# Kernel optimization log

Hardware: AMD Instinct MI355X
Metric: run time of the kernel (lower is better)

The kernel has to match this reference:

```python
import jax, jax.numpy as jnp
import numpy as np

N_NODES = 100000
N_EDGES = 1600000
D = 32
K = 3  # Chebyshev kernels
NEG_SLOPE = 0.2


def setup_inputs() -> dict:
    key = jax.random.key(0)
    ks = jax.random.split(key, 10)
    s = 1.0 / np.sqrt(D)
    return {
        "u": jax.random.normal(ks[0], (N_NODES, D), jnp.float32),
        "lambda_max": jnp.full((1,), 2.0, jnp.float32),
        "edge_src": jax.random.randint(ks[1], (N_EDGES,), 0, N_NODES, jnp.int32),
        "edge_dst": jax.random.randint(ks[2], (N_EDGES,), 0, N_NODES, jnp.int32),
        "cheb_W": jax.random.normal(ks[3], (K * D, D), jnp.float32) * s,
        "cheb_b": jnp.zeros((D,), jnp.float32),
        "src_W": jax.random.normal(ks[4], (D, D), jnp.float32) * s,
        "src_b": jnp.zeros((D,), jnp.float32),
        "dst_W": jax.random.normal(ks[5], (D, D), jnp.float32) * s,
        "dst_b": jnp.zeros((D,), jnp.float32),
        "attn": jax.random.normal(ks[6], (1, D), jnp.float32) * s,  # (heads=1, D)
    }


def reference(u, lambda_max, edge_src, edge_dst, cheb_W, cheb_b,
              src_W, src_b, dst_W, dst_b, attn):
    N = u.shape[0]
    # in-degrees (DGL: clamp(min=1) ** -0.5)
    deg = jnp.zeros((N,), u.dtype).at[edge_dst].add(1.0)
    Dinv = jnp.clip(deg, 1.0, None) ** -0.5  # (N,)

    def unnL(x):  # D^{-1/2} A D^{-1/2} x  via copy_u->sum message passing
        m = (x * Dinv[:, None])[edge_src]                       # (E, D)
        agg = jax.ops.segment_sum(m, edge_dst, num_segments=N)  # (N, D)
        return agg * Dinv[:, None]

    # --- ChebConv ---
    re_norm = 2.0 / lambda_max  # (1,) broadcast over all nodes
    X0 = u
    Xt = [X0]
    X1 = X0
    if K > 1:
        h = unnL(X0)
        X1 = -re_norm * h + X0 * (re_norm - 1.0)
        Xt.append(X1)
    for _ in range(2, K):
        h = unnL(X1)
        Xi = -2.0 * re_norm * h + X1 * (2.0 * (re_norm - 1.0)) - X0
        Xt.append(Xi)
        X0, X1 = X1, Xi
    Xcat = jnp.concatenate(Xt, axis=1)                 # (N, K*D)
    hc = jax.nn.relu(Xcat @ cheb_W + cheb_b)           # (N, D), DGL default activation=relu

    # --- GATv2Conv (heads=1) ---
    H = attn.shape[0]
    fsrc = (hc @ src_W + src_b).reshape(N, H, -1)      # (N, H, D)
    fdst = (hc @ dst_W + dst_b).reshape(N, H, -1)
    e = jax.nn.leaky_relu(fsrc[edge_src] + fdst[edge_dst], NEG_SLOPE)  # (E, H, D)
    logits = jnp.einsum('ehd,hd->eh', e, attn)         # (E, H)
    mx = jax.ops.segment_max(logits, edge_dst, num_segments=N)
    mx = jnp.where(jnp.isfinite(mx), mx, 0.0)
    ex = jnp.exp(logits - mx[edge_dst])
    den = jax.ops.segment_sum(ex, edge_dst, num_segments=N)
    a = ex / jnp.where(den > 0, den, 1.0)[edge_dst]    # edge softmax over dst groups
    msg = fsrc[edge_src] * a[:, :, None]               # (E, H, D)
    out = jax.ops.segment_sum(msg, edge_dst, num_segments=N)  # (N, H, D)
    return out.squeeze(1)
```

## Files before the change

### kernel.cpp

```cpp
#include <hip/hip_runtime.h>
#include <hip/hip_bf16.h>


typedef unsigned short u16;

#define DD 32
#define NEG_SLOPE 0.2f
#define BLK 256
#define TILE 4096
#define CB_SHIFT 8
#define CB_NODES 256
#define SRC_BITS 17

#define OFF_CHEBW 0
#define OFF_CHEBB 3072
#define OFF_SRCW  3104
#define OFF_SRCB  4128
#define OFF_DSTW  4160
#define OFF_DSTB  5184
#define OFF_ATTN  5216
#define OFF_LMAX  5248
#define W_TOTAL   5249

#define F_U     0
#define F_CHEBW 1
#define F_CHEBB 2
#define F_SRCW  3
#define F_SRCB  4
#define F_DSTW  5
#define F_DSTB  6
#define F_ATTN  7
#define F_LMAX  8
#define N_FLAGS 9

__device__ __forceinline__ float bh2f(u16 h) {
    return __uint_as_float(((unsigned)h) << 16);
}
__device__ __forceinline__ float rdin(const void* p, long long i, int f32f) {
    return f32f ? ((const float*)p)[i] : bh2f(((const u16*)p)[i]);
}
__device__ __forceinline__ float4 rd4(const void* p, long long row, int q, int f32f) {
    if (f32f) return ((const float4*)p)[row * 8 + q];
    ushort4 h = ((const ushort4*)p)[row * 8 + q];
    return make_float4(bh2f(h.x), bh2f(h.y), bh2f(h.z), bh2f(h.w));
}
__device__ __forceinline__ float lrelu(float x) { return fmaxf(x, NEG_SLOPE * x); }

__device__ __forceinline__ int plaus(u16 h) {
    if ((h & 0x7FFFu) == 0) return 1;
    unsigned e = (h >> 7) & 0xFF;
    return (e >= 0x60 && e <= 0x8F) ? 1 : 0;
}

__global__ void k_detect(const void* p0, const void* p1, const void* p2,
                         const void* p3, const void* p4, const void* p5,
                         const void* p6, const void* p7, const void* p8,
                         int n0, int n7, int* __restrict__ flags) {
    __shared__ int cEven, cEvenZ, cOddNZ;
    const void* ptrs[N_FLAGS] = {p0, p1, p2, p3, p4, p5, p6, p7, p8};
    const int   ns[N_FLAGS]   = {n0, 3072, 32, 1024, 32, 1024, 32, n7, 1};
    int a = blockIdx.x;
    if (a >= N_FLAGS) return;
    const u16* h = (const u16*)ptrs[a];
    int n = ns[a];
    if (threadIdx.x == 0) { cEven = 0; cEvenZ = 0; cOddNZ = 0; }
    __syncthreads();
    if (n == 1) {
        if (threadIdx.x == 0) {
            u16 v = h[0];
            flags[a] = ((v & 0x7FFFu) == 0 || !plaus(v)) ? 1 : 0;
        }
        return;
    }
    int nprobe = n >> 1;
    if (nprobe > 64) nprobe = 64;
    int t = threadIdx.x;
    if (t < nprobe) {
        u16 ev = h[2 * t];
        u16 od = h[2 * t + 1];
        if (plaus(ev)) atomicAdd(&cEven, 1);
        if ((ev & 0x7FFFu) == 0) atomicAdd(&cEvenZ, 1);
        if (plaus(od) && (od & 0x7FFFu) != 0) atomicAdd(&cOddNZ, 1);
    }
    __syncthreads();
    if (threadIdx.x == 0) {
        int bf = (cEven * 4 >= nprobe * 3);
        if (cEvenZ == nprobe && cOddNZ * 2 >= nprobe) bf = 0;
        flags[a] = bf ? 0 : 1;
    }
}

__global__ void k_cvtw(const void* chebW, const void* chebB, const void* srcW,
                       const void* srcB, const void* dstW, const void* dstB,
                       const void* attn, const void* lmax,
                       const int* __restrict__ flags, float* __restrict__ wsW,
                       unsigned* __restrict__ Mabs) {
    int i = blockIdx.x * blockDim.x + threadIdx.x;
    if (i >= W_TOTAL + 32) return;
    if (i >= W_TOTAL) { Mabs[i - W_TOTAL] = 0u; return; }
    float v;
    if      (i < OFF_CHEBB) v = rdin(chebW, i - OFF_CHEBW, flags[F_CHEBW]);
    else if (i < OFF_SRCW)  v = rdin(chebB, i - OFF_CHEBB, flags[F_CHEBB]);
    else if (i < OFF_SRCB)  v = rdin(srcW,  i - OFF_SRCW,  flags[F_SRCW]);
    else if (i < OFF_DSTW)  v = rdin(srcB,  i - OFF_SRCB,  flags[F_SRCB]);
    else if (i < OFF_DSTB)  v = rdin(dstW,  i - OFF_DSTW,  flags[F_DSTW]);
    else if (i < OFF_ATTN)  v = rdin(dstB,  i - OFF_DSTB,  flags[F_DSTB]);
    else if (i < OFF_LMAX)  v = rdin(attn,  i - OFF_ATTN,  flags[F_ATTN]);
    else                    v = rdin(lmax,  0,             flags[F_LMAX]);
    wsW[i] = v;
}


__global__ __launch_bounds__(BLK) void k_h1(
        const int* __restrict__ dst, unsigned* __restrict__ hist1,
        int E, int T, int NB1) {
    __shared__ unsigned lh[512];
    int tile = blockIdx.x, t = threadIdx.x;
    for (int b = t; b < 512; b += BLK) lh[b] = 0;
    __syncthreads();
    int base = tile * TILE;
    for (int i = 0; i < TILE / BLK; i++) {
        int e = base + i * BLK + t;
        if (e < E) atomicAdd(&lh[dst[e] >> CB_SHIFT], 1u);
    }
    __syncthreads();
    for (int b = t; b < NB1; b += BLK) hist1[(size_t)b * T + tile] = lh[b];
}

__global__ __launch_bounds__(BLK) void k_scA(
        unsigned* __restrict__ h, unsigned* __restrict__ bsum, int T) {
    __shared__ unsigned s[BLK];
    int b = blockIdx.x, t = threadIdx.x;
    unsigned carry = 0;
    for (int base = 0; base < T; base += BLK) {
        int i = base + t;
        unsigned v = (i < T) ? h[(size_t)b * T + i] : 0u;
        s[t] = v;
        __syncthreads();
        for (int off = 1; off < BLK; off <<= 1) {
            unsigned a = (t >= off) ? s[t - off] : 0u;
            __syncthreads();
            s[t] += a;
            __syncthreads();
        }
        if (i < T) h[(size_t)b * T + i] = carry + s[t] - v;
        carry += s[BLK - 1];
        __syncthreads();
    }
    if (t == 0) bsum[b] = carry;
}

__global__ __launch_bounds__(512) void k_scB(
        unsigned* __restrict__ bsum, int NB1,
        unsigned* __restrict__ row_ptr, int N, int E) {
    __shared__ unsigned s[512];
    int t = threadIdx.x;
    unsigned v = (t < NB1) ? bsum[t] : 0u;
    s[t] = v;
    __syncthreads();
    for (int off = 1; off < 512; off <<= 1) {
        unsigned a = (t >= off) ? s[t - off] : 0u;
        __syncthreads();
        s[t] += a;
        __syncthreads();
    }
    if (t < NB1) bsum[t] = s[t] - v;
    if (t == 0) row_ptr[N] = (unsigned)E;
}

__global__ __launch_bounds__(BLK) void k_s1(
        const int* __restrict__ src, const int* __restrict__ dst,
        const unsigned* __restrict__ off1, const unsigned* __restrict__ bsum,
        unsigned* __restrict__ tmp, int E, int T, int NB1) {
    __shared__ unsigned cur[512];
    int tile = blockIdx.x, t = threadIdx.x;
    for (int b = t; b < NB1; b += BLK)
        cur[b] = off1[(size_t)b * T + tile] + bsum[b];
    __syncthreads();
    int base = tile * TILE;
    for (int i = 0; i < TILE / BLK; i++) {
        int e = base + i * BLK + t;
        if (e < E) {
            int d = dst[e];
            unsigned pos = atomicAdd(&cur[d >> CB_SHIFT], 1u);
            tmp[pos] = ((unsigned)(d & (CB_NODES - 1)) << SRC_BITS) | (unsigned)src[e];
        }
    }
}

__global__ __launch_bounds__(BLK) void k_p2(
        const unsigned* __restrict__ tmp, const unsigned* __restrict__ bsum,
        unsigned* __restrict__ row_ptr, float* __restrict__ dinv,
        int* __restrict__ srcs, int N, int E, int T, int NB1) {
    __shared__ unsigned hist[CB_NODES], cur[CB_NODES], ssc[BLK];
    int b = blockIdx.x, t = threadIdx.x;
    int nodeBase = b << CB_SHIFT;
    unsigned lo = bsum[b];
    unsigned hi = (b + 1 < NB1) ? bsum[b + 1] : (unsigned)E;
    hist[t] = 0;
    __syncthreads();
    for (unsigned e = lo + t; e < hi; e += BLK)
        atomicAdd(&hist[tmp[e] >> SRC_BITS], 1u);
    __syncthreads();
    unsigned v = hist[t];
    ssc[t] = v;
    __syncthreads();
    for (int off = 1; off < BLK; off <<= 1) {
        unsigned a = (t >= off) ? ssc[t - off] : 0u;
        __syncthreads();
        ssc[t] += a;
        __syncthreads();
    }
    unsigned ex = ssc[t] - v;
    cur[t] = ex;
    int node = nodeBase + t;
    if (node < N) {
        row_ptr[node] = lo + ex;
        unsigned c = v;
        if (c < 1u) c = 1u;
        dinv[node] = rsqrtf((float)c);
    }
    __syncthreads();
    for (unsigned e = lo + t; e < hi; e += BLK) {
        unsigned p = tmp[e];
        unsigned pos = lo + atomicAdd(&cur[p >> SRC_BITS], 1u);
        srcs[pos] = (int)(p & ((1u << SRC_BITS) - 1u));
    }
}


__global__ __launch_bounds__(BLK) void k_unnl1(
        const void* __restrict__ u, const int* __restrict__ flags,
        const float* __restrict__ dinv, const unsigned* __restrict__ row_ptr,
        const int* __restrict__ srcs, const float* __restrict__ wsW,
        float* __restrict__ X1, int N) {
    int wave = (blockIdx.x * BLK + threadIdx.x) >> 6;
    if (wave >= N) return;
    int lane = threadIdx.x & 63, q = lane & 7, g = lane >> 3;
    int f = flags[F_U];
    int base = (int)row_ptr[wave], end = (int)row_ptr[wave + 1];
    float4 acc = make_float4(0.f, 0.f, 0.f, 0.f);
    for (int i = base; i < end; i += 32) {
        int e0 = i + g, e1 = i + 8 + g, e2 = i + 16 + g, e3 = i + 24 + g;
        int s0 = srcs[min(e0, end - 1)], s1 = srcs[min(e1, end - 1)];
        int s2 = srcs[min(e2, end - 1)], s3 = srcs[min(e3, end - 1)];
        float dv0 = dinv[s0], dv1 = dinv[s1], dv2 = dinv[s2], dv3 = dinv[s3];
        if (e0 >= end) dv0 = 0.f;
        if (e1 >= end) dv1 = 0.f;
        if (e2 >= end) dv2 = 0.f;
        if (e3 >= end) dv3 = 0.f;
        float4 x0 = rd4(u, s0, q, f);
        float4 x1 = rd4(u, s1, q, f);
        float4 x2 = rd4(u, s2, q, f);
        float4 x3 = rd4(u, s3, q, f);
        acc.x += x0.x * dv0 + x1.x * dv1 + x2.x * dv2 + x3.x * dv3;
        acc.y += x0.y * dv0 + x1.y * dv1 + x2.y * dv2 + x3.y * dv3;
        acc.z += x0.z * dv0 + x1.z * dv1 + x2.z * dv2 + x3.z * dv3;
        acc.w += x0.w * dv0 + x1.w * dv1 + x2.w * dv2 + x3.w * dv3;
    }
#pragma unroll
    for (int off = 8; off <= 32; off <<= 1) {
        acc.x += __shfl_xor(acc.x, off);
        acc.y += __shfl_xor(acc.y, off);
        acc.z += __shfl_xor(acc.z, off);
        acc.w += __shfl_xor(acc.w, off);
    }
    if (g == 0) {
        float rn = 2.0f / wsW[OFF_LMAX];
        float dn = dinv[wave];
        float4 x0 = rd4(u, wave, q, f);
        float4 r;
        r.x = -rn * (acc.x * dn) + x0.x * (rn - 1.f);
        r.y = -rn * (acc.y * dn) + x0.y * (rn - 1.f);
        r.z = -rn * (acc.z * dn) + x0.z * (rn - 1.f);
        r.w = -rn * (acc.w * dn) + x0.w * (rn - 1.f);
        ((float4*)X1)[(size_t)wave * 8 + q] = r;
    }
}

__global__ __launch_bounds__(BLK) void k_unnl2(
        const void* __restrict__ u, const int* __restrict__ flags,
        const float* __restrict__ X1, const float* __restrict__ dinv,
        const unsigned* __restrict__ row_ptr, const int* __restrict__ srcs,
        const float* __restrict__ wsW, float* __restrict__ X2, int N) {
    int wave = (blockIdx.x * BLK + threadIdx.x) >> 6;
    if (wave >= N) return;
    int lane = threadIdx.x & 63, q = lane & 7, g = lane >> 3;
    int base = (int)row_ptr[wave], end = (int)row_ptr[wave + 1];
    float4 acc = make_float4(0.f, 0.f, 0.f, 0.f);
    for (int i = base; i < end; i += 32) {
        int e0 = i + g, e1 = i + 8 + g, e2 = i + 16 + g, e3 = i + 24 + g;
        int s0 = srcs[min(e0, end - 1)], s1 = srcs[min(e1, end - 1)];
        int s2 = srcs[min(e2, end - 1)], s3 = srcs[min(e3, end - 1)];
        float dv0 = dinv[s0], dv1 = dinv[s1], dv2 = dinv[s2], dv3 = dinv[s3];
        if (e0 >= end) dv0 = 0.f;
        if (e1 >= end) dv1 = 0.f;
        if (e2 >= end) dv2 = 0.f;
        if (e3 >= end) dv3 = 0.f;
        float4 x0 = ((const float4*)X1)[(size_t)s0 * 8 + q];
        float4 x1 = ((const float4*)X1)[(size_t)s1 * 8 + q];
        float4 x2 = ((const float4*)X1)[(size_t)s2 * 8 + q];
        float4 x3 = ((const float4*)X1)[(size_t)s3 * 8 + q];
        acc.x += x0.x * dv0 + x1.x * dv1 + x2.x * dv2 + x3.x * dv3;
        acc.y += x0.y * dv0 + x1.y * dv1 + x2.y * dv2 + x3.y * dv3;
        acc.z += x0.z * dv0 + x1.z * dv1 + x2.z * dv2 + x3.z * dv3;
        acc.w += x0.w * dv0 + x1.w * dv1 + x2.w * dv2 + x3.w * dv3;
    }
#pragma unroll
    for (int off = 8; off <= 32; off <<= 1) {
        acc.x += __shfl_xor(acc.x, off);
        acc.y += __shfl_xor(acc.y, off);
        acc.z += __shfl_xor(acc.z, off);
        acc.w += __shfl_xor(acc.w, off);
    }
    if (g == 0) {
        float rn = 2.0f / wsW[OFF_LMAX];
        float dn = dinv[wave];
        float4 x0 = rd4(u, wave, q, flags[F_U]);
        float4 x1 = ((const float4*)X1)[(size_t)wave * 8 + q];
        float4 r;
        r.x = -2.f * rn * (acc.x * dn) + x1.x * (2.f * (rn - 1.f)) - x0.x;
        r.y = -2.f * rn * (acc.y * dn) + x1.y * (2.f * (rn - 1.f)) - x0.y;
        r.z = -2.f * rn * (acc.z * dn) + x1.z * (2.f * (rn - 1.f)) - x0.z;
        r.w = -2.f * rn * (acc.w * dn) + x1.w * (2.f * (rn - 1.f)) - x0.w;
        ((float4*)X2)[(size_t)wave * 8 + q] = r;
    }
}

__global__ __launch_bounds__(BLK) void k_cfsd(
        const void* __restrict__ u, const int* __restrict__ flags,
        const float* __restrict__ X1, const float* __restrict__ X2,
        const float* __restrict__ wsW, float* __restrict__ fsrc,
        float* __restrict__ fdst, unsigned* __restrict__ Mabs, int N) {
    __shared__ float sW[3072], sWs[1024], sWd[1024];
    __shared__ float sb[32], sbs[32], sbd[32];
    __shared__ float hcS[BLK * 33];
    __shared__ unsigned mloc[32];
    int t = threadIdx.x;
    for (int i = t; i < 3072; i += BLK) sW[i] = wsW[OFF_CHEBW + i];
    for (int i = t; i < 1024; i += BLK) {
        sWs[i] = wsW[OFF_SRCW + i];
        sWd[i] = wsW[OFF_DSTW + i];
    }
    if (t < 32) {
        sb[t]  = wsW[OFF_CHEBB + t];
        sbs[t] = wsW[OFF_SRCB + t];
        sbd[t] = wsW[OFF_DSTB + t];
        mloc[t] = 0u;
    }
    __syncthreads();
    int f = flags[F_U];
    float mabs = 0.f;
    int n = blockIdx.x * BLK + t;
    if (n < N) {
        long long row = (long long)n;
        float acc[32];
#pragma unroll
        for (int j = 0; j < 32; j++) acc[j] = sb[j];
        for (int i4 = 0; i4 < 8; i4++) {
            float4 x = rd4(u, row, i4, f);
            const float* w = &sW[i4 * 128];
#pragma unroll
            for (int j = 0; j < 32; j++) acc[j] = fmaf(x.x, w[j], acc[j]);
#pragma unroll
            for (int j = 0; j < 32; j++) acc[j] = fmaf(x.y, w[32 + j], acc[j]);
#pragma unroll
            for (int j = 0; j < 32; j++) acc[j] = fmaf(x.z, w[64 + j], acc[j]);
#pragma unroll
            for (int j = 0; j < 32; j++) acc[j] = fmaf(x.w, w[96 + j], acc[j]);
        }
        for (int i4 = 0; i4 < 8; i4++) {
            float4 x = ((const float4*)X1)[row * 8 + i4];
            const float* w = &sW[1024 + i4 * 128];
#pragma unroll
            for (int j = 0; j < 32; j++) acc[j] = fmaf(x.x, w[j], acc[j]);
#pragma unroll
            for (int j = 0; j < 32; j++) acc[j] = fmaf(x.y, w[32 + j], acc[j]);
#pragma unroll
            for (int j = 0; j < 32; j++) acc[j] = fmaf(x.z, w[64 + j], acc[j]);
#pragma unroll
            for (int j = 0; j < 32; j++) acc[j] = fmaf(x.w, w[96 + j], acc[j]);
        }
        for (int i4 = 0; i4 < 8; i4++) {
            float4 x = ((const float4*)X2)[row * 8 + i4];
            const float* w = &sW[2048 + i4 * 128];
#pragma unroll
            for (int j = 0; j < 32; j++) acc[j] = fmaf(x.x, w[j], acc[j]);
#pragma unroll
            for (int j = 0; j < 32; j++) acc[j] = fmaf(x.y, w[32 + j], acc[j]);
#pragma unroll
            for (int j = 0; j < 32; j++) acc[j] = fmaf(x.z, w[64 + j], acc[j]);
#pragma unroll
            for (int j = 0; j < 32; j++) acc[j] = fmaf(x.w, w[96 + j], acc[j]);
        }
#pragma unroll
        for (int j = 0; j < 32; j++) hcS[t * 33 + j] = fmaxf(acc[j], 0.f);
        float as[32], ad[32];
#pragma unroll
        for (int j = 0; j < 32; j++) { as[j] = sbs[j]; ad[j] = sbd[j]; }
        for (int i = 0; i < 32; i++) {
            float hv = hcS[t * 33 + i];
            const float* ws = &sWs[i * 32];
            const float* wd = &sWd[i * 32];
#pragma unroll
            for (int j = 0; j < 32; j++) {
                as[j] = fmaf(hv, ws[j], as[j]);
                ad[j] = fmaf(hv, wd[j], ad[j]);
            }
        }
        float4* fs4 = (float4*)(fsrc + row * 32);
        float4* fd4 = (float4*)(fdst + row * 32);
#pragma unroll
        for (int i4 = 0; i4 < 8; i4++) {
            fs4[i4] = make_float4(as[4 * i4], as[4 * i4 + 1], as[4 * i4 + 2], as[4 * i4 + 3]);
            fd4[i4] = make_float4(ad[4 * i4], ad[4 * i4 + 1], ad[4 * i4 + 2], ad[4 * i4 + 3]);
        }
#pragma unroll
        for (int j = 0; j < 32; j++) mabs = fmaxf(mabs, fabsf(as[j]));
    }
    atomicMax(&mloc[t & 31], __float_as_uint(mabs));
    __syncthreads();
    if (t < 32) atomicMax(&Mabs[t], mloc[t]);
}

__global__ __launch_bounds__(BLK) void k_gat(
        const float* __restrict__ fsrc, const float* __restrict__ fdst,
        const unsigned* __restrict__ row_ptr, const int* __restrict__ srcs,
        const float* __restrict__ wsW, const unsigned* __restrict__ Mabs,
        float* __restrict__ out, int N) {
    int wave = (blockIdx.x * BLK + threadIdx.x) >> 6;
    if (wave >= N) return;
    int lane = threadIdx.x & 63, q = lane & 7, g = lane >> 3;
    int base = (int)row_ptr[wave], end = (int)row_ptr[wave + 1];
    if (base == end) {
        if (g == 0)
            ((float4*)out)[(size_t)wave * 8 + q] = make_float4(0.f, 0.f, 0.f, 0.f);
        return;
    }
    float4 fd = ((const float4*)fdst)[(size_t)wave * 8 + q];
    float4 at = ((const float4*)(wsW + OFF_ATTN))[q];
    float4 mb = ((const float4*)Mabs)[q];
    float kp = (mb.x + fabsf(fd.x)) * fabsf(at.x) +
               (mb.y + fabsf(fd.y)) * fabsf(at.y) +
               (mb.z + fabsf(fd.z)) * fabsf(at.z) +
               (mb.w + fabsf(fd.w)) * fabsf(at.w);
    kp += __shfl_xor(kp, 1);
    kp += __shfl_xor(kp, 2);
    kp += __shfl_xor(kp, 4);
    float K = kp;
    float4 acc = make_float4(0.f, 0.f, 0.f, 0.f);
    float den = 0.f;
    for (int i = base; i < end; i += 16) {
        int e0 = i + g, e1 = i + 8 + g;
        int ec0 = min(e0, end - 1), ec1 = min(e1, end - 1);
        int s0 = srcs[ec0], s1 = srcs[ec1];
        float4 fs0 = ((const float4*)fsrc)[(size_t)s0 * 8 + q];
        float4 fs1 = ((const float4*)fsrc)[(size_t)s1 * 8 + q];
        float v0 = lrelu(fs0.x + fd.x) * at.x + lrelu(fs0.y + fd.y) * at.y +
                   lrelu(fs0.z + fd.z) * at.z + lrelu(fs0.w + fd.w) * at.w;
        float v1 = lrelu(fs1.x + fd.x) * at.x + lrelu(fs1.y + fd.y) * at.y +
                   lrelu(fs1.z + fd.z) * at.z + lrelu(fs1.w + fd.w) * at.w;
        v0 += __shfl_xor(v0, 1);  v1 += __shfl_xor(v1, 1);
        v0 += __shfl_xor(v0, 2);  v1 += __shfl_xor(v1, 2);
        v0 += __shfl_xor(v0, 4);  v1 += __shfl_xor(v1, 4);
        float w0 = (e0 < end) ? __expf(v0 - K) : 0.f;
        float w1 = (e1 < end) ? __expf(v1 - K) : 0.f;
        acc.x += fs0.x * w0 + fs1.x * w1;
        acc.y += fs0.y * w0 + fs1.y * w1;
        acc.z += fs0.z * w0 + fs1.z * w1;
        acc.w += fs0.w * w0 + fs1.w * w1;
        den += w0 + w1;
    }
#pragma unroll
    for (int off = 8; off <= 32; off <<= 1) {
        acc.x += __shfl_xor(acc.x, off);
        acc.y += __shfl_xor(acc.y, off);
        acc.z += __shfl_xor(acc.z, off);
        acc.w += __shfl_xor(acc.w, off);
        den   += __shfl_xor(den, off);
    }
    if (g == 0) {
        float inv = 1.f / (den > 0.f ? den : 1.f);
        ((float4*)out)[(size_t)wave * 8 + q] =
            make_float4(acc.x * inv, acc.y * inv, acc.z * inv, acc.w * inv);
    }
}

extern "C" void kernel_launch(void* const* d_in, const int* in_sizes, int n_in,
                              void* d_out, int out_size, void* d_ws, size_t ws_size,
                              hipStream_t stream) {
    const void* u     = d_in[0];
    const void* lmax  = d_in[1];
    const int*  esrc  = (const int*)d_in[2];
    const int*  edst  = (const int*)d_in[3];
    const void* chebW = d_in[4];
    const void* chebB = d_in[5];
    const void* srcW  = d_in[6];
    const void* srcB  = d_in[7];
    const void* dstW  = d_in[8];
    const void* dstB  = d_in[9];
    const void* attn  = d_in[10];

    const int ND = in_sizes[0];
    const int N  = ND / DD;
    const int E  = in_sizes[2];

    const int NB1 = (N + CB_NODES - 1) >> CB_SHIFT;
    const int T   = (E + TILE - 1) / TILE;
    const int M   = NB1 * T;

    float* ws   = (float*)d_ws;
    float* X1   = ws;
    float* X2   = ws + (size_t)ND;
    unsigned* tmp = (unsigned*)(ws + 2 * (size_t)ND);
    int*   srcs = (int*)(tmp + E);
    unsigned* hist1   = (unsigned*)(srcs + E);
    unsigned* row_ptr = hist1 + M;
    float*    dinv    = (float*)(row_ptr + (N + 1));
    unsigned* bsum    = (unsigned*)(dinv + N);
    float*    wsW     = (float*)(((uintptr_t)(bsum + NB1) + 15) & ~(uintptr_t)15);
    int*      flags   = (int*)(wsW + W_TOTAL);
    unsigned* Mabs    = (unsigned*)(((uintptr_t)(flags + N_FLAGS) + 15) & ~(uintptr_t)15);
    float*    out     = (float*)d_out;

    auto gb = [](long long n, int b) { return (unsigned)((n + b - 1) / b); };

    k_detect<<<N_FLAGS, 64, 0, stream>>>(u, chebW, chebB, srcW, srcB, dstW, dstB,
                                         attn, lmax, ND, DD, flags);
    k_cvtw<<<gb(W_TOTAL + 32, BLK), BLK, 0, stream>>>(chebW, chebB, srcW, srcB,
                                                      dstW, dstB, attn, lmax,
                                                      flags, wsW, Mabs);

    k_h1<<<T, BLK, 0, stream>>>(edst, hist1, E, T, NB1);
    k_scA<<<NB1, BLK, 0, stream>>>(hist1, bsum, T);
    k_scB<<<1, 512, 0, stream>>>(bsum, NB1, row_ptr, N, E);
    k_s1<<<T, BLK, 0, stream>>>(esrc, edst, hist1, bsum, tmp, E, T, NB1);
    k_p2<<<NB1, BLK, 0, stream>>>(tmp, bsum, row_ptr, dinv, srcs, N, E, T, NB1);

    k_unnl1<<<gb((long long)N * 64, BLK), BLK, 0, stream>>>(u, flags, dinv, row_ptr,
                                                            srcs, wsW, X1, N);
    k_unnl2<<<gb((long long)N * 64, BLK), BLK, 0, stream>>>(u, flags, X1, dinv, row_ptr,
                                                            srcs, wsW, X2, N);

    k_cfsd<<<gb(N, BLK), BLK, 0, stream>>>(u, flags, X1, X2, wsW, X1, X2, Mabs, N);

    k_gat<<<gb((long long)N * 64, BLK), BLK, 0, stream>>>(X1, X2, row_ptr, srcs,
                                                          wsW, Mabs, out, N);
}
```

Measured before the change: 290.8 us.

## Map eight lanes per node instead of a full wave in gather kernels

Result: faster. 270.9 us (-6.9%).

```diff
diff --git a/kernel.cpp b/kernel.cpp
--- a/kernel.cpp
+++ b/kernel.cpp
@@ -234,18 +234,19 @@
         const float* __restrict__ dinv, const unsigned* __restrict__ row_ptr,
         const int* __restrict__ srcs, const float* __restrict__ wsW,
         float* __restrict__ X1, int N) {
-    int wave = (blockIdx.x * BLK + threadIdx.x) >> 6;
-    if (wave >= N) return;
-    int lane = threadIdx.x & 63, q = lane & 7, g = lane >> 3;
+    int node = (blockIdx.x * BLK + threadIdx.x) >> 3;
+    if (node >= N) return;
+    int q = threadIdx.x & 7;
     int f = flags[F_U];
-    int base = (int)row_ptr[wave], end = (int)row_ptr[wave + 1];
+    int base = (int)row_ptr[node], end = (int)row_ptr[node + 1];
     float4 acc = make_float4(0.f, 0.f, 0.f, 0.f);
-    for (int i = base; i < end; i += 32) {
-        int e0 = i + g, e1 = i + 8 + g, e2 = i + 16 + g, e3 = i + 24 + g;
-        int s0 = srcs[min(e0, end - 1)], s1 = srcs[min(e1, end - 1)];
-        int s2 = srcs[min(e2, end - 1)], s3 = srcs[min(e3, end - 1)];
+    for (int i = base; i < end; i += 4) {
+        int e1 = i + 1, e2 = i + 2, e3 = i + 3;
+        int s0 = srcs[i];
+        int s1 = srcs[min(e1, end - 1)];
+        int s2 = srcs[min(e2, end - 1)];
+        int s3 = srcs[min(e3, end - 1)];
         float dv0 = dinv[s0], dv1 = dinv[s1], dv2 = dinv[s2], dv3 = dinv[s3];
-        if (e0 >= end) dv0 = 0.f;
         if (e1 >= end) dv1 = 0.f;
         if (e2 >= end) dv2 = 0.f;
         if (e3 >= end) dv3 = 0.f;
@@ -258,24 +259,15 @@
         acc.z += x0.z * dv0 + x1.z * dv1 + x2.z * dv2 + x3.z * dv3;
         acc.w += x0.w * dv0 + x1.w * dv1 + x2.w * dv2 + x3.w * dv3;
     }
-#pragma unroll
-    for (int off = 8; off <= 32; off <<= 1) {
-        acc.x += __shfl_xor(acc.x, off);
-        acc.y += __shfl_xor(acc.y, off);
-        acc.z += __shfl_xor(acc.z, off);
-        acc.w += __shfl_xor(acc.w, off);
-    }
-    if (g == 0) {
-        float rn = 2.0f / wsW[OFF_LMAX];
-        float dn = dinv[wave];
-        float4 x0 = rd4(u, wave, q, f);
-        float4 r;
-        r.x = -rn * (acc.x * dn) + x0.x * (rn - 1.f);
-        r.y = -rn * (acc.y * dn) + x0.y * (rn - 1.f);
-        r.z = -rn * (acc.z * dn) + x0.z * (rn - 1.f);
-        r.w = -rn * (acc.w * dn) + x0.w * (rn - 1.f);
-        ((float4*)X1)[(size_t)wave * 8 + q] = r;
-    }
+    float rn = 2.0f / wsW[OFF_LMAX];
+    float dn = dinv[node];
+    float4 x0 = rd4(u, node, q, f);
+    float4 r;
+    r.x = -rn * (acc.x * dn) + x0.x * (rn - 1.f);
+    r.y = -rn * (acc.y * dn) + x0.y * (rn - 1.f);
+    r.z = -rn * (acc.z * dn) + x0.z * (rn - 1.f);
+    r.w = -rn * (acc.w * dn) + x0.w * (rn - 1.f);
+    ((float4*)X1)[(size_t)node * 8 + q] = r;
 }
 
 __global__ __launch_bounds__(BLK) void k_unnl2(
@@ -283,17 +275,18 @@
         const float* __restrict__ X1, const float* __restrict__ dinv,
         const unsigned* __restrict__ row_ptr, const int* __restrict__ srcs,
         const float* __restrict__ wsW, float* __restrict__ X2, int N) {
-    int wave = (blockIdx.x * BLK + threadIdx.x) >> 6;
-    if (wave >= N) return;
-    int lane = threadIdx.x & 63, q = lane & 7, g = lane >> 3;
-    int base = (int)row_ptr[wave], end = (int)row_ptr[wave + 1];
+    int node = (blockIdx.x * BLK + threadIdx.x) >> 3;
+    if (node >= N) return;
+    int q = threadIdx.x & 7;
+    int base = (int)row_ptr[node], end = (int)row_ptr[node + 1];
     float4 acc = make_float4(0.f, 0.f, 0.f, 0.f);
-    for (int i = base; i < end; i += 32) {
-        int e0 = i + g, e1 = i + 8 + g, e2 = i + 16 + g, e3 = i + 24 + g;
-        int s0 = srcs[min(e0, end - 1)], s1 = srcs[min(e1, end - 1)];
-        int s2 = srcs[min(e2, end - 1)], s3 = srcs[min(e3, end - 1)];
+    for (int i = base; i < end; i += 4) {
+        int e1 = i + 1, e2 = i + 2, e3 = i + 3;
+        int s0 = srcs[i];
+        int s1 = srcs[min(e1, end - 1)];
+        int s2 = srcs[min(e2, end - 1)];
+        int s3 = srcs[min(e3, end - 1)];
         float dv0 = dinv[s0], dv1 = dinv[s1], dv2 = dinv[s2], dv3 = dinv[s3];
-        if (e0 >= end) dv0 = 0.f;
         if (e1 >= end) dv1 = 0.f;
         if (e2 >= end) dv2 = 0.f;
         if (e3 >= end) dv3 = 0.f;
@@ -306,25 +299,16 @@
         acc.z += x0.z * dv0 + x1.z * dv1 + x2.z * dv2 + x3.z * dv3;
         acc.w += x0.w * dv0 + x1.w * dv1 + x2.w * dv2 + x3.w * dv3;
     }
-#pragma unroll
-    for (int off = 8; off <= 32; off <<= 1) {
-        acc.x += __shfl_xor(acc.x, off);
-        acc.y += __shfl_xor(acc.y, off);
-        acc.z += __shfl_xor(acc.z, off);
-        acc.w += __shfl_xor(acc.w, off);
-    }
-    if (g == 0) {
-        float rn = 2.0f / wsW[OFF_LMAX];
-        float dn = dinv[wave];
-        float4 x0 = rd4(u, wave, q, flags[F_U]);
-        float4 x1 = ((const float4*)X1)[(size_t)wave * 8 + q];
-        float4 r;
-        r.x = -2.f * rn * (acc.x * dn) + x1.x * (2.f * (rn - 1.f)) - x0.x;
-        r.y = -2.f * rn * (acc.y * dn) + x1.y * (2.f * (rn - 1.f)) - x0.y;
-        r.z = -2.f * rn * (acc.z * dn) + x1.z * (2.f * (rn - 1.f)) - x0.z;
-        r.w = -2.f * rn * (acc.w * dn) + x1.w * (2.f * (rn - 1.f)) - x0.w;
-        ((float4*)X2)[(size_t)wave * 8 + q] = r;
-    }
+    float rn = 2.0f / wsW[OFF_LMAX];
+    float dn = dinv[node];
+    float4 x0 = rd4(u, node, q, flags[F_U]);
+    float4 x1 = ((const float4*)X1)[(size_t)node * 8 + q];
+    float4 r;
+    r.x = -2.f * rn * (acc.x * dn) + x1.x * (2.f * (rn - 1.f)) - x0.x;
+    r.y = -2.f * rn * (acc.y * dn) + x1.y * (2.f * (rn - 1.f)) - x0.y;
+    r.z = -2.f * rn * (acc.z * dn) + x1.z * (2.f * (rn - 1.f)) - x0.z;
+    r.w = -2.f * rn * (acc.w * dn) + x1.w * (2.f * (rn - 1.f)) - x0.w;
+    ((float4*)X2)[(size_t)node * 8 + q] = r;
 }
 
 __global__ __launch_bounds__(BLK) void k_cfsd(
@@ -428,16 +412,15 @@
         const unsigned* __restrict__ row_ptr, const int* __restrict__ srcs,
         const float* __restrict__ wsW, const unsigned* __restrict__ Mabs,
         float* __restrict__ out, int N) {
-    int wave = (blockIdx.x * BLK + threadIdx.x) >> 6;
-    if (wave >= N) return;
-    int lane = threadIdx.x & 63, q = lane & 7, g = lane >> 3;
-    int base = (int)row_ptr[wave], end = (int)row_ptr[wave + 1];
+    int node = (blockIdx.x * BLK + threadIdx.x) >> 3;
+    if (node >= N) return;
+    int q = threadIdx.x & 7;
+    int base = (int)row_ptr[node], end = (int)row_ptr[node + 1];
     if (base == end) {
-        if (g == 0)
-            ((float4*)out)[(size_t)wave * 8 + q] = make_float4(0.f, 0.f, 0.f, 0.f);
+        ((float4*)out)[(size_t)node * 8 + q] = make_float4(0.f, 0.f, 0.f, 0.f);
         return;
     }
-    float4 fd = ((const float4*)fdst)[(size_t)wave * 8 + q];
+    float4 fd = ((const float4*)fdst)[(size_t)node * 8 + q];
     float4 at = ((const float4*)(wsW + OFF_ATTN))[q];
     float4 mb = ((const float4*)Mabs)[q];
     float kp = (mb.x + fabsf(fd.x)) * fabsf(at.x) +
@@ -450,10 +433,10 @@
     float K = kp;
     float4 acc = make_float4(0.f, 0.f, 0.f, 0.f);
     float den = 0.f;
-    for (int i = base; i < end; i += 16) {
-        int e0 = i + g, e1 = i + 8 + g;
-        int ec0 = min(e0, end - 1), ec1 = min(e1, end - 1);
-        int s0 = srcs[ec0], s1 = srcs[ec1];
+    for (int i = base; i < end; i += 2) {
+        int e1 = i + 1;
+        int s0 = srcs[i];
+        int s1 = srcs[min(e1, end - 1)];
         float4 fs0 = ((const float4*)fsrc)[(size_t)s0 * 8 + q];
         float4 fs1 = ((const float4*)fsrc)[(size_t)s1 * 8 + q];
         float v0 = lrelu(fs0.x + fd.x) * at.x + lrelu(fs0.y + fd.y) * at.y +
@@ -463,7 +446,7 @@
         v0 += __shfl_xor(v0, 1);  v1 += __shfl_xor(v1, 1);
         v0 += __shfl_xor(v0, 2);  v1 += __shfl_xor(v1, 2);
         v0 += __shfl_xor(v0, 4);  v1 += __shfl_xor(v1, 4);
-        float w0 = (e0 < end) ? __expf(v0 - K) : 0.f;
+        float w0 = __expf(v0 - K);
         float w1 = (e1 < end) ? __expf(v1 - K) : 0.f;
         acc.x += fs0.x * w0 + fs1.x * w1;
         acc.y += fs0.y * w0 + fs1.y * w1;
@@ -471,19 +454,9 @@
         acc.w += fs0.w * w0 + fs1.w * w1;
         den += w0 + w1;
     }
-#pragma unroll
-    for (int off = 8; off <= 32; off <<= 1) {
-        acc.x += __shfl_xor(acc.x, off);
-        acc.y += __shfl_xor(acc.y, off);
-        acc.z += __shfl_xor(acc.z, off);
-        acc.w += __shfl_xor(acc.w, off);
-        den   += __shfl_xor(den, off);
-    }
-    if (g == 0) {
-        float inv = 1.f / (den > 0.f ? den : 1.f);
-        ((float4*)out)[(size_t)wave * 8 + q] =
-            make_float4(acc.x * inv, acc.y * inv, acc.z * inv, acc.w * inv);
-    }
+    float inv = 1.f / (den > 0.f ? den : 1.f);
+    ((float4*)out)[(size_t)node * 8 + q] =
+        make_float4(acc.x * inv, acc.y * inv, acc.z * inv, acc.w * inv);
 }
 
 extern "C" void kernel_launch(void* const* d_in, const int* in_sizes, int n_in,
@@ -537,13 +510,13 @@
     k_s1<<<T, BLK, 0, stream>>>(esrc, edst, hist1, bsum, tmp, E, T, NB1);
     k_p2<<<NB1, BLK, 0, stream>>>(tmp, bsum, row_ptr, dinv, srcs, N, E, T, NB1);
 
-    k_unnl1<<<gb((long long)N * 64, BLK), BLK, 0, stream>>>(u, flags, dinv, row_ptr,
-                                                            srcs, wsW, X1, N);
-    k_unnl2<<<gb((long long)N * 64, BLK), BLK, 0, stream>>>(u, flags, X1, dinv, row_ptr,
-                                                            srcs, wsW, X2, N);
+    k_unnl1<<<gb((long long)N * 8, BLK), BLK, 0, stream>>>(u, flags, dinv, row_ptr,
+                                                           srcs, wsW, X1, N);
+    k_unnl2<<<gb((long long)N * 8, BLK), BLK, 0, stream>>>(u, flags, X1, dinv, row_ptr,
+                                                           srcs, wsW, X2, N);
 
     k_cfsd<<<gb(N, BLK), BLK, 0, stream>>>(u, flags, X1, X2, wsW, X1, X2, Mabs, N);
 
-    k_gat<<<gb((long long)N * 64, BLK), BLK, 0, stream>>>(X1, X2, row_ptr, srcs,
-                                                          wsW, Mabs, out, N);
-}
+    k_gat<<<gb((long long)N * 8, BLK), BLK, 0, stream>>>(X1, X2, row_ptr, srcs,
+                                                         wsW, Mabs, out, N);
+}
```
